# Optimization experiments

Measured on AMD Instinct MI355X. Metric: run time of the kernel, lower is better.

The kernel has to match this reference:

```python
import jax, jax.numpy as jnp
import numpy as np

EPS = 1e-5
N0, K1, K2 = 1000, 500, 100  # node counts fixed by the view() calls in the source


def _conv_bn_relu(x, w, b, g, be):
    # Conv1d(k=1) == per-node linear; BatchNorm1d in training mode over nodes
    h = x @ w.T + b                      # (N, Cout)
    mu = h.mean(0)
    var = h.var(0)                       # biased variance, as torch BN uses
    return jax.nn.relu(g * (h - mu) * jax.lax.rsqrt(var + EPS) + be)


def _linear_relu(x, w, b):
    return jax.nn.relu(x @ w.T + b)


def _sag_pool(x, src, dst, ew, w_rel, w_root, bias, k):
    # SAGPooling with GraphConv scorer (sum aggregation weighted by edge_attr)
    N = x.shape[0]
    agg = jax.ops.segment_sum(ew[:, None] * x[src], dst, num_segments=N)  # (N, C)
    score = agg @ w_rel + x @ w_root + bias                               # (N,)
    top_s, perm = jax.lax.top_k(score, k)
    xk = x[perm] * jnp.tanh(top_s)[:, None]                               # (k, C)
    # re-index edges: keep only edges between surviving nodes (mask, fixed E)
    new_idx = jnp.zeros(N, jnp.int32).at[perm].set(jnp.arange(k, dtype=jnp.int32))
    keep = jnp.zeros(N, bool).at[perm].set(True)
    valid = keep[src] & keep[dst]
    nsrc = jnp.where(valid, new_idx[src], 0)
    ndst = jnp.where(valid, new_idx[dst], 0)
    new_ew = jnp.where(valid, ew, 0.0)  # zero weight == edge removed
    return xk, nsrc, ndst, new_ew


def setup_inputs() -> dict:
    key = jax.random.key(0)
    ks = jax.random.split(key, 32)
    nrm = lambda k, sh, s=0.05: jax.random.normal(k, sh, jnp.float32) * s
    E = 32000
    return {
        "x": jax.random.normal(ks[0], (1, N0, 3), jnp.float32),
        "edge_index": jax.random.randint(ks[1], (2, E), 0, N0, jnp.int32),
        "edge_attr": jax.random.uniform(ks[2], (E,), jnp.float32),
        # input: Conv1d(3,64)+BN
        "w0": nrm(ks[3], (64, 3)), "b0": jnp.zeros(64), "g0": jnp.ones(64), "be0": jnp.zeros(64),
        # mlp_first: Conv1d(64,64)+BN
        "w1": nrm(ks[4], (64, 64)), "b1": jnp.zeros(64), "g1": jnp.ones(64), "be1": jnp.zeros(64),
        # mlp_second: Conv1d(64,128)+BN, Conv1d(128,200)+BN
        "w2a": nrm(ks[5], (128, 64)), "b2a": jnp.zeros(128), "g2a": jnp.ones(128), "be2a": jnp.zeros(128),
        "w2b": nrm(ks[6], (200, 128)), "b2b": jnp.zeros(200), "g2b": jnp.ones(200), "be2b": jnp.zeros(200),
        # mlp_third: Conv1d(200,128), Conv1d(128,2) (no BN)
        "w3a": nrm(ks[7], (128, 200)), "b3a": jnp.zeros(128),
        "w3b": nrm(ks[8], (2, 128)), "b3b": jnp.zeros(2),
        # SAGPooling scorers (GraphConv(in_channels, 1))
        "p1_wrel": nrm(ks[9], (64,)), "p1_wroot": nrm(ks[10], (64,)), "p1_b": jnp.zeros(()),
        "p2_wrel": nrm(ks[11], (200,)), "p2_wroot": nrm(ks[12], (200,)), "p2_b": jnp.zeros(()),
    }


def reference(x, edge_index, edge_attr,
              w0, b0, g0, be0, w1, b1, g1, be1,
              w2a, b2a, g2a, be2a, w2b, b2b, g2b, be2b,
              w3a, b3a, w3b, b3b,
              p1_wrel, p1_wroot, p1_b, p2_wrel, p2_wroot, p2_b):
    h = x.reshape(N0, 3)
    src, dst = edge_index[0], edge_index[1]
    ew = edge_attr.reshape(-1)

    h = _conv_bn_relu(h, w0, b0, g0, be0)      # (1000, 64)
    h = _conv_bn_relu(h, w1, b1, g1, be1)      # (1000, 64)
    h, src, dst, ew = _sag_pool(h, src, dst, ew, p1_wrel, p1_wroot, p1_b, K1)

    h = _conv_bn_relu(h, w2a, b2a, g2a, be2a)  # (500, 128)
    h = _conv_bn_relu(h, w2b, b2b, g2b, be2b)  # (500, 200)
    h, src, dst, ew = _sag_pool(h, src, dst, ew, p2_wrel, p2_wroot, p2_b, K2)

    g = h.max(0)                               # global max pool over 100 nodes -> (200,)
    h3 = _linear_relu(g, w3a, b3a)             # (128,)
    out = _linear_relu(h3, w3b, b3b)           # (2,)
    return jax.nn.log_softmax(out)[None, :]    # (1, 2)
```

## Files before the change

kernel.cpp:

```cpp
#include <hip/hip_runtime.h>
#include <math.h>

#define EPS 1e-5f
#define N0 1000
#define K1 500
#define K2 100
#define NE 32000

__device__ __forceinline__ float bnr(float h, float sc, float sh) {
    float v = fmaf(h, sc, sh);
    return v > 0.f ? v : 0.f;
}

__global__ void k_lin0(const float* __restrict__ x, const float* __restrict__ w0,
                       const float* __restrict__ b0, float* __restrict__ h0,
                       float* __restrict__ psum0) {
    int t = threadIdx.x;
    int c = t & 63, ns = t >> 6;
    int nb = blockIdx.x * 128;
    float wa = w0[c * 3 + 0], wb = w0[c * 3 + 1], wc = w0[c * 3 + 2], bb = b0[c];
    float s = 0.f, q = 0.f;
    for (int j = 0; j < 32; ++j) {
        int n = nb + ns + 4 * j;
        if (n < N0) {
            float h = fmaf(wa, x[n * 3], fmaf(wb, x[n * 3 + 1], fmaf(wc, x[n * 3 + 2], bb)));
            h0[n * 64 + c] = h;
            s += h; q += h * h;
        }
    }
    __shared__ float rs[256], rq[256];
    rs[t] = s; rq[t] = q;
    __syncthreads();
    if (ns == 0) {
        psum0[blockIdx.x * 128 + c]      = rs[c] + rs[c + 64] + rs[c + 128] + rs[c + 192];
        psum0[blockIdx.x * 128 + 64 + c] = rq[c] + rq[c + 64] + rq[c + 128] + rq[c + 192];
    }
}

__global__ void k_lin1(const float* __restrict__ h0, const float* __restrict__ w1,
                       const float* __restrict__ b1v, const float* __restrict__ g0,
                       const float* __restrict__ be0, const float* __restrict__ psum0,
                       float* __restrict__ h1, float* __restrict__ psum1) {
    __shared__ float xs[64][65];
    __shared__ float wsm[64][65];
    __shared__ float sc0[64], sh0[64];
    __shared__ float rs[256], rq[256];
    int t = threadIdx.x;
    int nb = blockIdx.x * 64;
    if (t < 64) {
        float s = 0.f, q = 0.f;
        for (int i = 0; i < 8; ++i) { s += psum0[i * 128 + t]; q += psum0[i * 128 + 64 + t]; }
        float mu = s * (1.f / N0);
        float var = q * (1.f / N0) - mu * mu;
        float sc = g0[t] * rsqrtf(var + EPS);
        sc0[t] = sc; sh0[t] = be0[t] - mu * sc;
    }
    __syncthreads();
    for (int i = 0; i < 16; ++i) {
        int e = t + i * 256;
        int r = e >> 6, cc = e & 63;
        int n = nb + r;
        xs[r][cc] = (n < N0) ? bnr(h0[n * 64 + cc], sc0[cc], sh0[cc]) : 0.f;
        wsm[r][cc] = w1[e];
    }
    __syncthreads();
    int c = t & 63, ns = t >> 6;
    float s = 0.f, q = 0.f;
    for (int j = 0; j < 16; ++j) {
        int ln = ns + 4 * j;
        int n = nb + ln;
        if (n < N0) {
            float acc = b1v[c];
            #pragma unroll
            for (int k = 0; k < 64; ++k) acc = fmaf(xs[ln][k], wsm[c][k], acc);
            h1[n * 64 + c] = acc;
            s += acc; q += acc * acc;
        }
    }
    rs[t] = s; rq[t] = q;
    __syncthreads();
    if (ns == 0) {
        psum1[blockIdx.x * 128 + c]      = rs[c] + rs[c + 64] + rs[c + 128] + rs[c + 192];
        psum1[blockIdx.x * 128 + 64 + c] = rq[c] + rq[c + 64] + rq[c + 128] + rq[c + 192];
    }
}

__global__ void k_score1(const float* __restrict__ h1, const float* __restrict__ psum1,
                         const float* __restrict__ g1, const float* __restrict__ be1,
                         const float* __restrict__ wrel, const float* __restrict__ wroot,
                         const float* __restrict__ pb,
                         float* __restrict__ t1, float* __restrict__ sc1) {
    __shared__ float sc[64], sh[64];
    int t = threadIdx.x;
    if (t < 64) {
        float s = 0.f, q = 0.f;
        for (int i = 0; i < 16; ++i) { s += psum1[i * 128 + t]; q += psum1[i * 128 + 64 + t]; }
        float mu = s * (1.f / N0);
        float var = q * (1.f / N0) - mu * mu;
        float sv = g1[t] * rsqrtf(var + EPS);
        sc[t] = sv; sh[t] = be1[t] - mu * sv;
    }
    __syncthreads();
    int lane = t & 63, w = t >> 6;
    int n = blockIdx.x * 4 + w;
    if (n < N0) {
        float v = bnr(h1[n * 64 + lane], sc[lane], sh[lane]);
        float dr = v * wrel[lane], dt = v * wroot[lane];
        #pragma unroll
        for (int m = 32; m >= 1; m >>= 1) {
            dr += __shfl_xor(dr, m, 64);
            dt += __shfl_xor(dt, m, 64);
        }
        if (lane == 0) { t1[n] = dr; sc1[n] = dt + pb[0]; }
    }
}

__global__ void k_scatter1(const int* __restrict__ ei, const float* __restrict__ ea,
                           const float* __restrict__ t1, float* __restrict__ sc1) {
    __shared__ float acc[N0];
    int t = threadIdx.x;
    for (int i = t; i < N0; i += 256) acc[i] = 0.f;
    __syncthreads();
    for (int e = blockIdx.x * 256 + t; e < NE; e += gridDim.x * 256) {
        float w = ea[e];
        if (w != 0.f) atomicAdd(&acc[ei[NE + e]], w * t1[ei[e]]);
    }
    __syncthreads();
    for (int i = t; i < N0; i += 256) {
        float v = acc[i];
        if (v != 0.f) atomicAdd(&sc1[i], v);
    }
}

__global__ void k_rank1(const float* __restrict__ sc1, const float* __restrict__ h1,
                        const float* __restrict__ psum1, const float* __restrict__ g1,
                        const float* __restrict__ be1,
                        float* __restrict__ xp1, int* __restrict__ keep, int* __restrict__ nidx) {
    __shared__ float ss[N0];
    __shared__ float sc[64], sh[64];
    int t = threadIdx.x;
    if (t < 64) {
        float s = 0.f, q = 0.f;
        for (int i = 0; i < 16; ++i) { s += psum1[i * 128 + t]; q += psum1[i * 128 + 64 + t]; }
        float mu = s * (1.f / N0);
        float var = q * (1.f / N0) - mu * mu;
        float sv = g1[t] * rsqrtf(var + EPS);
        sc[t] = sv; sh[t] = be1[t] - mu * sv;
    }
    for (int i = t; i < N0; i += 256) ss[i] = sc1[i];
    __syncthreads();
    int lane = t & 63, w = t >> 6;
    int n = blockIdx.x * 4 + w;
    if (n < N0) {
        float s = ss[n];
        int r = 0;
        for (int m = lane; m < N0; m += 64) {
            float sm = ss[m];
            r += (sm > s) || (sm == s && m < n);
        }
        #pragma unroll
        for (int msk = 32; msk >= 1; msk >>= 1) r += __shfl_xor(r, msk, 64);
        if (lane == 0) { keep[n] = (r < K1) ? 1 : 0; nidx[n] = (r < K1) ? r : 0; }
        if (r < K1) {
            float tn = tanhf(s);
            xp1[r * 64 + lane] = bnr(h1[n * 64 + lane], sc[lane], sh[lane]) * tn;
        }
    }
}

__global__ void k_lin2a_remap(const float* __restrict__ xp1, const float* __restrict__ w2a,
                              const float* __restrict__ b2a, float* __restrict__ h2a,
                              float* __restrict__ psum2a,
                              const int* __restrict__ ei, const float* __restrict__ ea,
                              const int* __restrict__ keep, const int* __restrict__ nidx,
                              int* __restrict__ nsrc, int* __restrict__ ndst,
                              float* __restrict__ new_ew) {
    __shared__ float xs[64][65];
    __shared__ float wsm[128][65];
    __shared__ float rs[256], rq[256];
    int b = blockIdx.x;
    int t = threadIdx.x;
    if (b < 8) {
        int nb = b * 64;
        for (int i = 0; i < 16; ++i) {
            int e = t + i * 256;
            int r = e >> 6, cc = e & 63;
            int n = nb + r;
            xs[r][cc] = (n < K1) ? xp1[n * 64 + cc] : 0.f;
        }
        for (int i = 0; i < 32; ++i) {
            int e = t + i * 256;
            wsm[e >> 6][e & 63] = w2a[e];
        }
        __syncthreads();
        int c = t & 127, ns = t >> 7;
        float s = 0.f, q = 0.f;
        for (int j = 0; j < 32; ++j) {
            int ln = ns + 2 * j;
            int n = nb + ln;
            if (n < K1) {
                float acc = b2a[c];
                #pragma unroll
                for (int k = 0; k < 64; ++k) acc = fmaf(xs[ln][k], wsm[c][k], acc);
                h2a[n * 128 + c] = acc;
                s += acc; q += acc * acc;
            }
        }
        rs[t] = s; rq[t] = q;
        __syncthreads();
        if (ns == 0) {
            psum2a[b * 256 + c]       = rs[c] + rs[c + 128];
            psum2a[b * 256 + 128 + c] = rq[c] + rq[c + 128];
        }
    } else {
        int e = (b - 8) * 256 + t;
        if (e < NE) {
            int s = ei[e], d = ei[NE + e];
            bool v = keep[s] && keep[d];
            nsrc[e] = v ? nidx[s] : 0;
            ndst[e] = v ? nidx[d] : 0;
            new_ew[e] = v ? ea[e] : 0.f;
        }
    }
}

__global__ void k_lin2b(const float* __restrict__ h2a, const float* __restrict__ psum2a,
                        const float* __restrict__ g2a, const float* __restrict__ be2a,
                        const float* __restrict__ w2b, const float* __restrict__ b2b,
                        float* __restrict__ h2b, float* __restrict__ psum2b) {
    __shared__ float wsm[200][33];
    __shared__ float xs[25][33];
    __shared__ float sc[128], sh[128];
    int t = threadIdx.x;
    if (t < 128) {
        float s = 0.f, q = 0.f;
        for (int i = 0; i < 8; ++i) { s += psum2a[i * 256 + t]; q += psum2a[i * 256 + 128 + t]; }
        float mu = s * (1.f / K1);
        float var = q * (1.f / K1) - mu * mu;
        float sv = g2a[t] * rsqrtf(var + EPS);
        sc[t] = sv; sh[t] = be2a[t] - mu * sv;
    }
    __syncthreads();
    int nb = blockIdx.x * 25;
    float acc[25];
    if (t < 200) {
        float bb = b2b[t];
        #pragma unroll
        for (int r = 0; r < 25; ++r) acc[r] = bb;
    }
    for (int kt = 0; kt < 4; ++kt) {
        int k0 = kt * 32;
        __syncthreads();
        for (int e = t; e < 200 * 32; e += 256) {
            int r = e >> 5, k = e & 31;
            wsm[r][k] = w2b[r * 128 + k0 + k];
        }
        for (int e = t; e < 25 * 32; e += 256) {
            int r = e >> 5, k = e & 31;
            int n = nb + r;
            xs[r][k] = bnr(h2a[n * 128 + k0 + k], sc[k0 + k], sh[k0 + k]);
        }
        __syncthreads();
        if (t < 200) {
            for (int k = 0; k < 32; ++k) {
                float wv = wsm[t][k];
                #pragma unroll
                for (int r = 0; r < 25; ++r) acc[r] = fmaf(xs[r][k], wv, acc[r]);
            }
        }
    }
    if (t < 200) {
        float s = 0.f, q = 0.f;
        #pragma unroll
        for (int r = 0; r < 25; ++r) {
            int n = nb + r;
            h2b[n * 200 + t] = acc[r];
            s += acc[r]; q += acc[r] * acc[r];
        }
        psum2b[blockIdx.x * 400 + t]       = s;
        psum2b[blockIdx.x * 400 + 200 + t] = q;
    }
}

__global__ void k_score2(const float* __restrict__ h2b, const float* __restrict__ psum2b,
                         const float* __restrict__ g2b, const float* __restrict__ be2b,
                         const float* __restrict__ wrel, const float* __restrict__ wroot,
                         const float* __restrict__ pb,
                         float* __restrict__ t2, float* __restrict__ sc2) {
    __shared__ float sc[200], sh[200];
    int t = threadIdx.x;
    if (t < 200) {
        float s = 0.f, q = 0.f;
        for (int i = 0; i < 20; ++i) { s += psum2b[i * 400 + t]; q += psum2b[i * 400 + 200 + t]; }
        float mu = s * (1.f / K1);
        float var = q * (1.f / K1) - mu * mu;
        float sv = g2b[t] * rsqrtf(var + EPS);
        sc[t] = sv; sh[t] = be2b[t] - mu * sv;
    }
    __syncthreads();
    int lane = t & 63, w = t >> 6;
    int n = blockIdx.x * 4 + w;
    if (n < K1) {
        float dr = 0.f, dt = 0.f;
        #pragma unroll
        for (int j = 0; j < 4; ++j) {
            int ch = lane + 64 * j;
            if (ch < 200) {
                float v = bnr(h2b[n * 200 + ch], sc[ch], sh[ch]);
                dr = fmaf(v, wrel[ch], dr);
                dt = fmaf(v, wroot[ch], dt);
            }
        }
        #pragma unroll
        for (int m = 32; m >= 1; m >>= 1) {
            dr += __shfl_xor(dr, m, 64);
            dt += __shfl_xor(dt, m, 64);
        }
        if (lane == 0) { t2[n] = dr; sc2[n] = dt + pb[0]; }
    }
}

__global__ void k_scatter2(const int* __restrict__ nsrc, const int* __restrict__ ndst,
                           const float* __restrict__ new_ew, const float* __restrict__ t2,
                           float* __restrict__ sc2) {
    __shared__ float acc[K1];
    int t = threadIdx.x;
    for (int i = t; i < K1; i += 256) acc[i] = 0.f;
    __syncthreads();
    for (int e = blockIdx.x * 256 + t; e < NE; e += gridDim.x * 256) {
        float w = new_ew[e];
        if (w != 0.f) atomicAdd(&acc[ndst[e]], w * t2[nsrc[e]]);
    }
    __syncthreads();
    for (int i = t; i < K1; i += 256) {
        float v = acc[i];
        if (v != 0.f) atomicAdd(&sc2[i], v);
    }
}

__global__ void k_rank2(const float* __restrict__ sc2v, const float* __restrict__ h2b,
                        const float* __restrict__ psum2b, const float* __restrict__ g2b,
                        const float* __restrict__ be2b, float* __restrict__ xp2) {
    __shared__ float ss[K1];
    __shared__ float sc[200], sh[200];
    int t = threadIdx.x;
    if (t < 200) {
        float s = 0.f, q = 0.f;
        for (int i = 0; i < 20; ++i) { s += psum2b[i * 400 + t]; q += psum2b[i * 400 + 200 + t]; }
        float mu = s * (1.f / K1);
        float var = q * (1.f / K1) - mu * mu;
        float sv = g2b[t] * rsqrtf(var + EPS);
        sc[t] = sv; sh[t] = be2b[t] - mu * sv;
    }
    for (int i = t; i < K1; i += 256) ss[i] = sc2v[i];
    __syncthreads();
    int lane = t & 63, w = t >> 6;
    int n = blockIdx.x * 4 + w;
    if (n < K1) {
        float s = ss[n];
        int r = 0;
        for (int m = lane; m < K1; m += 64) {
            float sm = ss[m];
            r += (sm > s) || (sm == s && m < n);
        }
        #pragma unroll
        for (int msk = 32; msk >= 1; msk >>= 1) r += __shfl_xor(r, msk, 64);
        if (r < K2) {
            float tn = tanhf(s);
            #pragma unroll
            for (int j = 0; j < 4; ++j) {
                int ch = lane + 64 * j;
                if (ch < 200)
                    xp2[r * 200 + ch] = bnr(h2b[n * 200 + ch], sc[ch], sh[ch]) * tn;
            }
        }
    }
}

__global__ void k_final(const float* __restrict__ xp2, const float* __restrict__ w3a,
                        const float* __restrict__ b3a, const float* __restrict__ w3b,
                        const float* __restrict__ b3b, float* __restrict__ out) {
    __shared__ float g[200];
    __shared__ float buf[64][201];
    __shared__ float part[256];
    __shared__ float h3[128];
    __shared__ float o[2];
    int t = threadIdx.x;
    if (t < 200) {
        float m = -1e30f;
        for (int n = 0; n < K2; ++n) m = fmaxf(m, xp2[n * 200 + t]);
        g[t] = m;
    }
    __syncthreads();
    int lane = t & 63, q = t >> 6;
    for (int chunk = 0; chunk < 2; ++chunk) {
        int r0 = chunk * 64;
        __syncthreads();
        for (int e = t; e < 64 * 200; e += 256) {
            int r = e / 200, j = e - r * 200;
            buf[r][j] = w3a[r0 * 200 + e];
        }
        __syncthreads();
        float p = 0.f;
        for (int j = q * 50; j < q * 50 + 50; ++j) p = fmaf(buf[lane][j], g[j], p);
        part[t] = p;
        __syncthreads();
        if (t < 64) {
            float a = part[t] + part[t + 64] + part[t + 128] + part[t + 192] + b3a[r0 + t];
            h3[r0 + t] = fmaxf(a, 0.f);
        }
    }
    __syncthreads();
    if (t < 128) {
        int ow = t >> 6;
        float p = w3b[ow * 128 + lane] * h3[lane] + w3b[ow * 128 + 64 + lane] * h3[64 + lane];
        #pragma unroll
        for (int m = 32; m >= 1; m >>= 1) p += __shfl_xor(p, m, 64);
        if (lane == 0) o[ow] = fmaxf(p + b3b[ow], 0.f);
    }
    __syncthreads();
    if (t == 0) {
        float m = fmaxf(o[0], o[1]);
        float l = m + logf(expf(o[0] - m) + expf(o[1] - m));
        out[0] = o[0] - l;
        out[1] = o[1] - l;
    }
}

extern "C" void kernel_launch(void* const* d_in, const int* in_sizes, int n_in,
                              void* d_out, int out_size, void* d_ws, size_t ws_size,
                              hipStream_t stream) {
    const float* x    = (const float*)d_in[0];
    const int*   ei   = (const int*)d_in[1];
    const float* ea   = (const float*)d_in[2];
    const float* w0   = (const float*)d_in[3];
    const float* b0   = (const float*)d_in[4];
    const float* g0   = (const float*)d_in[5];
    const float* be0  = (const float*)d_in[6];
    const float* w1   = (const float*)d_in[7];
    const float* b1   = (const float*)d_in[8];
    const float* g1   = (const float*)d_in[9];
    const float* be1  = (const float*)d_in[10];
    const float* w2a  = (const float*)d_in[11];
    const float* b2a  = (const float*)d_in[12];
    const float* g2a  = (const float*)d_in[13];
    const float* be2a = (const float*)d_in[14];
    const float* w2b  = (const float*)d_in[15];
    const float* b2b  = (const float*)d_in[16];
    const float* g2b  = (const float*)d_in[17];
    const float* be2b = (const float*)d_in[18];
    const float* w3a  = (const float*)d_in[19];
    const float* b3a  = (const float*)d_in[20];
    const float* w3b  = (const float*)d_in[21];
    const float* b3b  = (const float*)d_in[22];
    const float* p1_wrel  = (const float*)d_in[23];
    const float* p1_wroot = (const float*)d_in[24];
    const float* p1_b     = (const float*)d_in[25];
    const float* p2_wrel  = (const float*)d_in[26];
    const float* p2_wroot = (const float*)d_in[27];
    const float* p2_b     = (const float*)d_in[28];

    float* ws = (float*)d_ws;
    float* h0     = ws;
    float* h1     = ws + 64000;
    float* psum0  = ws + 128000;
    float* psum1  = ws + 129024;
    float* psum2a = ws + 131072;
    float* psum2b = ws + 133120;
    float* t1     = ws + 141120;
    float* sc1    = ws + 142120;
    float* xp1    = ws + 143120;
    float* h2a    = ws + 175120;
    float* h2b    = ws + 239120;
    float* t2     = ws + 339120;
    float* sc2    = ws + 339620;
    float* xp2    = ws + 340120;
    int*   keep   = (int*)(ws + 360120);
    int*   nidx   = (int*)(ws + 361120);
    int*   nsrc   = (int*)(ws + 362120);
    int*   ndst   = (int*)(ws + 394120);
    float* new_ew = ws + 426120;

    float* out = (float*)d_out;

    k_lin0<<<8, 256, 0, stream>>>(x, w0, b0, h0, psum0);
    k_lin1<<<16, 256, 0, stream>>>(h0, w1, b1, g0, be0, psum0, h1, psum1);
    k_score1<<<250, 256, 0, stream>>>(h1, psum1, g1, be1, p1_wrel, p1_wroot, p1_b, t1, sc1);
    k_scatter1<<<16, 256, 0, stream>>>(ei, ea, t1, sc1);
    k_rank1<<<250, 256, 0, stream>>>(sc1, h1, psum1, g1, be1, xp1, keep, nidx);
    k_lin2a_remap<<<133, 256, 0, stream>>>(xp1, w2a, b2a, h2a, psum2a,
                                           ei, ea, keep, nidx, nsrc, ndst, new_ew);
    k_lin2b<<<20, 256, 0, stream>>>(h2a, psum2a, g2a, be2a, w2b, b2b, h2b, psum2b);
    k_score2<<<125, 256, 0, stream>>>(h2b, psum2b, g2b, be2b, p2_wrel, p2_wroot, p2_b, t2, sc2);
    k_scatter2<<<16, 256, 0, stream>>>(nsrc, ndst, new_ew, t2, sc2);
    k_rank2<<<125, 256, 0, stream>>>(sc2, h2b, psum2b, g2b, be2b, xp2);
    k_final<<<1, 256, 0, stream>>>(xp2, w3a, b3a, w3b, b3b, out);
}
```

Baseline: 130.3 us.

## Fuse graph pipeline into four kernels with redundant per-block pooling

Collapses eleven kernel launches into four. Each block of the first kernel recomputes the layer-0 batch-norm statistics itself. Each of the eight blocks in the pool1+lin2a kernel redundantly computes scores, edge scatter and ranking for all nodes in shared memory, then does its slice of the edge remap and the lin2a GEMM. The second pooling, ranking, global max and MLP head all run in one 1024-thread block. This removes launch overhead and global round-trips, but adds duplicated work across blocks and a serial O(N²) per-thread rank loop.

```diff
diff --git a/kernel.cpp b/kernel.cpp
--- a/kernel.cpp
+++ b/kernel.cpp
@@ -3,8 +3,8 @@
 
 #define EPS 1e-5f
 #define N0 1000
-#define K1 500
-#define K2 100
+#define NK1 500
+#define NK2 100
 #define NE 32000
 
 __device__ __forceinline__ float bnr(float h, float sc, float sh) {
@@ -12,65 +12,61 @@
     return v > 0.f ? v : 0.f;
 }
 
-__global__ void k_lin0(const float* __restrict__ x, const float* __restrict__ w0,
-                       const float* __restrict__ b0, float* __restrict__ h0,
-                       float* __restrict__ psum0) {
-    int t = threadIdx.x;
-    int c = t & 63, ns = t >> 6;
-    int nb = blockIdx.x * 128;
-    float wa = w0[c * 3 + 0], wb = w0[c * 3 + 1], wc = w0[c * 3 + 2], bb = b0[c];
-    float s = 0.f, q = 0.f;
-    for (int j = 0; j < 32; ++j) {
-        int n = nb + ns + 4 * j;
-        if (n < N0) {
-            float h = fmaf(wa, x[n * 3], fmaf(wb, x[n * 3 + 1], fmaf(wc, x[n * 3 + 2], bb)));
-            h0[n * 64 + c] = h;
-            s += h; q += h * h;
-        }
-    }
-    __shared__ float rs[256], rq[256];
-    rs[t] = s; rq[t] = q;
-    __syncthreads();
-    if (ns == 0) {
-        psum0[blockIdx.x * 128 + c]      = rs[c] + rs[c + 64] + rs[c + 128] + rs[c + 192];
-        psum0[blockIdx.x * 128 + 64 + c] = rq[c] + rq[c + 64] + rq[c + 128] + rq[c + 192];
-    }
-}
-
-__global__ void k_lin1(const float* __restrict__ h0, const float* __restrict__ w1,
-                       const float* __restrict__ b1v, const float* __restrict__ g0,
-                       const float* __restrict__ be0, const float* __restrict__ psum0,
-                       float* __restrict__ h1, float* __restrict__ psum1) {
-    __shared__ float xs[64][65];
-    __shared__ float wsm[64][65];
+__global__ __launch_bounds__(256) void k_lin01(
+        const float* __restrict__ x, const float* __restrict__ w0,
+        const float* __restrict__ b0, const float* __restrict__ g0,
+        const float* __restrict__ be0, const float* __restrict__ w1,
+        const float* __restrict__ b1, float* __restrict__ h1,
+        float* __restrict__ psum1) {
+    __shared__ float xs[64][65], wsm[64][65];
     __shared__ float sc0[64], sh0[64];
     __shared__ float rs[256], rq[256];
-    int t = threadIdx.x;
-    int nb = blockIdx.x * 64;
-    if (t < 64) {
+    const int t = threadIdx.x, b = blockIdx.x;
+    const int c = t & 63, ns = t >> 6;
+    const int nb = b * 64;
+
+    {
+        float wa = w0[c * 3], wb = w0[c * 3 + 1], wc = w0[c * 3 + 2], bb = b0[c];
         float s = 0.f, q = 0.f;
-        for (int i = 0; i < 8; ++i) { s += psum0[i * 128 + t]; q += psum0[i * 128 + 64 + t]; }
-        float mu = s * (1.f / N0);
-        float var = q * (1.f / N0) - mu * mu;
-        float sc = g0[t] * rsqrtf(var + EPS);
-        sc0[t] = sc; sh0[t] = be0[t] - mu * sc;
-    }
-    __syncthreads();
+        for (int n = ns; n < N0; n += 4) {
+            float h = fmaf(wa, x[n * 3], fmaf(wb, x[n * 3 + 1], fmaf(wc, x[n * 3 + 2], bb)));
+            s += h; q += h * h;
+        }
+        rs[t] = s; rq[t] = q;
+        __syncthreads();
+        if (ns == 0) {
+            float S = rs[c] + rs[c + 64] + rs[c + 128] + rs[c + 192];
+            float Q = rq[c] + rq[c + 64] + rq[c + 128] + rq[c + 192];
+            float mu = S * (1.f / N0);
+            float var = Q * (1.f / N0) - mu * mu;
+            float sv = g0[c] * rsqrtf(var + EPS);
+            sc0[c] = sv; sh0[c] = be0[c] - mu * sv;
+        }
+        __syncthreads();
+    }
+
     for (int i = 0; i < 16; ++i) {
         int e = t + i * 256;
         int r = e >> 6, cc = e & 63;
         int n = nb + r;
-        xs[r][cc] = (n < N0) ? bnr(h0[n * 64 + cc], sc0[cc], sh0[cc]) : 0.f;
+        float v = 0.f;
+        if (n < N0) {
+            float h = fmaf(w0[cc * 3], x[n * 3],
+                      fmaf(w0[cc * 3 + 1], x[n * 3 + 1],
+                      fmaf(w0[cc * 3 + 2], x[n * 3 + 2], b0[cc])));
+            v = bnr(h, sc0[cc], sh0[cc]);
+        }
+        xs[r][cc] = v;
         wsm[r][cc] = w1[e];
     }
     __syncthreads();
-    int c = t & 63, ns = t >> 6;
+
     float s = 0.f, q = 0.f;
     for (int j = 0; j < 16; ++j) {
         int ln = ns + 4 * j;
         int n = nb + ln;
         if (n < N0) {
-            float acc = b1v[c];
+            float acc = b1[c];
             #pragma unroll
             for (int k = 0; k < 64; ++k) acc = fmaf(xs[ln][k], wsm[c][k], acc);
             h1[n * 64 + c] = acc;
@@ -80,154 +76,131 @@
     rs[t] = s; rq[t] = q;
     __syncthreads();
     if (ns == 0) {
-        psum1[blockIdx.x * 128 + c]      = rs[c] + rs[c + 64] + rs[c + 128] + rs[c + 192];
-        psum1[blockIdx.x * 128 + 64 + c] = rq[c] + rq[c + 64] + rq[c + 128] + rq[c + 192];
-    }
-}
-
-__global__ void k_score1(const float* __restrict__ h1, const float* __restrict__ psum1,
-                         const float* __restrict__ g1, const float* __restrict__ be1,
-                         const float* __restrict__ wrel, const float* __restrict__ wroot,
-                         const float* __restrict__ pb,
-                         float* __restrict__ t1, float* __restrict__ sc1) {
-    __shared__ float sc[64], sh[64];
-    int t = threadIdx.x;
+        psum1[b * 128 + c]      = rs[c] + rs[c + 64] + rs[c + 128] + rs[c + 192];
+        psum1[b * 128 + 64 + c] = rq[c] + rq[c + 64] + rq[c + 128] + rq[c + 192];
+    }
+}
+
+__global__ __launch_bounds__(1024) void k_pool1_lin2a(
+        const float* __restrict__ h1, const float* __restrict__ psum1,
+        const float* __restrict__ g1, const float* __restrict__ be1,
+        const float* __restrict__ wrel, const float* __restrict__ wroot,
+        const float* __restrict__ pb,
+        const int* __restrict__ ei, const float* __restrict__ ea,
+        const float* __restrict__ w2a, const float* __restrict__ b2a,
+        float* __restrict__ h2a, float* __restrict__ psum2a,
+        int* __restrict__ nsrc, int* __restrict__ ndst,
+        float* __restrict__ new_ew) {
+    union U {
+        struct { float ss[N0], tt[N0], acc[N0]; int rk[N0]; } A;
+        struct { float xs[64][65], wsm[128][65], rs[1024], rq[1024]; } C;
+    };
+    __shared__ U u;
+    __shared__ float bsc[64], bsh[64];
+    __shared__ int pn[NK1];
+    __shared__ float th[NK1];
+    const int t = threadIdx.x, b = blockIdx.x;
+    const int lane = t & 63, w = t >> 6;
+
     if (t < 64) {
         float s = 0.f, q = 0.f;
         for (int i = 0; i < 16; ++i) { s += psum1[i * 128 + t]; q += psum1[i * 128 + 64 + t]; }
         float mu = s * (1.f / N0);
         float var = q * (1.f / N0) - mu * mu;
         float sv = g1[t] * rsqrtf(var + EPS);
-        sc[t] = sv; sh[t] = be1[t] - mu * sv;
-    }
-    __syncthreads();
-    int lane = t & 63, w = t >> 6;
-    int n = blockIdx.x * 4 + w;
-    if (n < N0) {
-        float v = bnr(h1[n * 64 + lane], sc[lane], sh[lane]);
+        bsc[t] = sv; bsh[t] = be1[t] - mu * sv;
+    }
+    for (int i = t; i < N0; i += 1024) u.A.acc[i] = 0.f;
+    __syncthreads();
+
+    for (int n = w; n < N0; n += 16) {
+        float v = bnr(h1[n * 64 + lane], bsc[lane], bsh[lane]);
         float dr = v * wrel[lane], dt = v * wroot[lane];
         #pragma unroll
         for (int m = 32; m >= 1; m >>= 1) {
             dr += __shfl_xor(dr, m, 64);
             dt += __shfl_xor(dt, m, 64);
         }
-        if (lane == 0) { t1[n] = dr; sc1[n] = dt + pb[0]; }
-    }
-}
-
-__global__ void k_scatter1(const int* __restrict__ ei, const float* __restrict__ ea,
-                           const float* __restrict__ t1, float* __restrict__ sc1) {
-    __shared__ float acc[N0];
-    int t = threadIdx.x;
-    for (int i = t; i < N0; i += 256) acc[i] = 0.f;
-    __syncthreads();
-    for (int e = blockIdx.x * 256 + t; e < NE; e += gridDim.x * 256) {
-        float w = ea[e];
-        if (w != 0.f) atomicAdd(&acc[ei[NE + e]], w * t1[ei[e]]);
-    }
-    __syncthreads();
-    for (int i = t; i < N0; i += 256) {
-        float v = acc[i];
-        if (v != 0.f) atomicAdd(&sc1[i], v);
-    }
-}
-
-__global__ void k_rank1(const float* __restrict__ sc1, const float* __restrict__ h1,
-                        const float* __restrict__ psum1, const float* __restrict__ g1,
-                        const float* __restrict__ be1,
-                        float* __restrict__ xp1, int* __restrict__ keep, int* __restrict__ nidx) {
-    __shared__ float ss[N0];
-    __shared__ float sc[64], sh[64];
-    int t = threadIdx.x;
-    if (t < 64) {
-        float s = 0.f, q = 0.f;
-        for (int i = 0; i < 16; ++i) { s += psum1[i * 128 + t]; q += psum1[i * 128 + 64 + t]; }
-        float mu = s * (1.f / N0);
-        float var = q * (1.f / N0) - mu * mu;
-        float sv = g1[t] * rsqrtf(var + EPS);
-        sc[t] = sv; sh[t] = be1[t] - mu * sv;
-    }
-    for (int i = t; i < N0; i += 256) ss[i] = sc1[i];
-    __syncthreads();
-    int lane = t & 63, w = t >> 6;
-    int n = blockIdx.x * 4 + w;
-    if (n < N0) {
-        float s = ss[n];
+        if (lane == 0) { u.A.tt[n] = dr; u.A.ss[n] = dt + pb[0]; }
+    }
+    __syncthreads();
+
+    for (int e = t; e < NE; e += 1024) {
+        float ew = ea[e];
+        if (ew != 0.f) atomicAdd(&u.A.acc[ei[NE + e]], ew * u.A.tt[ei[e]]);
+    }
+    __syncthreads();
+    for (int i = t; i < N0; i += 1024) u.A.ss[i] += u.A.acc[i];
+    __syncthreads();
+
+    if (t < N0) {
+        float s = u.A.ss[t];
         int r = 0;
-        for (int m = lane; m < N0; m += 64) {
-            float sm = ss[m];
-            r += (sm > s) || (sm == s && m < n);
-        }
-        #pragma unroll
-        for (int msk = 32; msk >= 1; msk >>= 1) r += __shfl_xor(r, msk, 64);
-        if (lane == 0) { keep[n] = (r < K1) ? 1 : 0; nidx[n] = (r < K1) ? r : 0; }
-        if (r < K1) {
-            float tn = tanhf(s);
-            xp1[r * 64 + lane] = bnr(h1[n * 64 + lane], sc[lane], sh[lane]) * tn;
-        }
-    }
-}
-
-__global__ void k_lin2a_remap(const float* __restrict__ xp1, const float* __restrict__ w2a,
-                              const float* __restrict__ b2a, float* __restrict__ h2a,
-                              float* __restrict__ psum2a,
-                              const int* __restrict__ ei, const float* __restrict__ ea,
-                              const int* __restrict__ keep, const int* __restrict__ nidx,
-                              int* __restrict__ nsrc, int* __restrict__ ndst,
-                              float* __restrict__ new_ew) {
-    __shared__ float xs[64][65];
-    __shared__ float wsm[128][65];
-    __shared__ float rs[256], rq[256];
-    int b = blockIdx.x;
-    int t = threadIdx.x;
-    if (b < 8) {
-        int nb = b * 64;
-        for (int i = 0; i < 16; ++i) {
-            int e = t + i * 256;
-            int r = e >> 6, cc = e & 63;
-            int n = nb + r;
-            xs[r][cc] = (n < K1) ? xp1[n * 64 + cc] : 0.f;
-        }
-        for (int i = 0; i < 32; ++i) {
-            int e = t + i * 256;
-            wsm[e >> 6][e & 63] = w2a[e];
-        }
-        __syncthreads();
-        int c = t & 127, ns = t >> 7;
-        float s = 0.f, q = 0.f;
-        for (int j = 0; j < 32; ++j) {
-            int ln = ns + 2 * j;
-            int n = nb + ln;
-            if (n < K1) {
-                float acc = b2a[c];
-                #pragma unroll
-                for (int k = 0; k < 64; ++k) acc = fmaf(xs[ln][k], wsm[c][k], acc);
-                h2a[n * 128 + c] = acc;
-                s += acc; q += acc * acc;
-            }
-        }
-        rs[t] = s; rq[t] = q;
-        __syncthreads();
-        if (ns == 0) {
-            psum2a[b * 256 + c]       = rs[c] + rs[c + 128];
-            psum2a[b * 256 + 128 + c] = rq[c] + rq[c + 128];
-        }
-    } else {
-        int e = (b - 8) * 256 + t;
-        if (e < NE) {
-            int s = ei[e], d = ei[NE + e];
-            bool v = keep[s] && keep[d];
-            nsrc[e] = v ? nidx[s] : 0;
-            ndst[e] = v ? nidx[d] : 0;
-            new_ew[e] = v ? ea[e] : 0.f;
-        }
-    }
-}
-
-__global__ void k_lin2b(const float* __restrict__ h2a, const float* __restrict__ psum2a,
-                        const float* __restrict__ g2a, const float* __restrict__ be2a,
-                        const float* __restrict__ w2b, const float* __restrict__ b2b,
-                        float* __restrict__ h2b, float* __restrict__ psum2b) {
+        for (int m = 0; m < N0; ++m) {
+            float smv = u.A.ss[m];
+            r += (smv > s) || (smv == s && m < t);
+        }
+        u.A.rk[t] = r;
+        if (r < NK1) { pn[r] = t; th[r] = tanhf(s); }
+    }
+    __syncthreads();
+
+    for (int e = b * 4000 + t; e < (b + 1) * 4000; e += 1024) {
+        int s_ = ei[e], d_ = ei[NE + e];
+        int rs_ = u.A.rk[s_], rd_ = u.A.rk[d_];
+        bool v = (rs_ < NK1) && (rd_ < NK1);
+        nsrc[e] = v ? rs_ : 0;
+        ndst[e] = v ? rd_ : 0;
+        new_ew[e] = v ? ea[e] : 0.f;
+    }
+    __syncthreads();
+
+    const int nb = b * 63;
+    const int nrows = (NK1 - nb) < 63 ? (NK1 - nb) : 63;
+    for (int idx = t; idx < 64 * 64; idx += 1024) {
+        int r = idx >> 6, c = idx & 63;
+        float v = 0.f;
+        if (r < nrows) {
+            int n = pn[nb + r];
+            v = bnr(h1[n * 64 + c], bsc[c], bsh[c]) * th[nb + r];
+        }
+        u.C.xs[r][c] = v;
+    }
+    for (int idx = t; idx < 128 * 64; idx += 1024) {
+        int c = idx >> 6, k = idx & 63;
+        u.C.wsm[c][k] = w2a[idx];
+    }
+    __syncthreads();
+
+    const int c = t & 127, slot = t >> 7;
+    float s = 0.f, q = 0.f;
+    #pragma unroll
+    for (int j = 0; j < 8; ++j) {
+        int r = slot + 8 * j;
+        if (r < nrows) {
+            float acc = b2a[c];
+            #pragma unroll
+            for (int k = 0; k < 64; ++k) acc = fmaf(u.C.xs[r][k], u.C.wsm[c][k], acc);
+            h2a[(nb + r) * 128 + c] = acc;
+            s += acc; q += acc * acc;
+        }
+    }
+    u.C.rs[t] = s; u.C.rq[t] = q;
+    __syncthreads();
+    if (slot == 0) {
+        float S = 0.f, Q = 0.f;
+        #pragma unroll
+        for (int j = 0; j < 8; ++j) { S += u.C.rs[c + 128 * j]; Q += u.C.rq[c + 128 * j]; }
+        psum2a[b * 256 + c]       = S;
+        psum2a[b * 256 + 128 + c] = Q;
+    }
+}
+
+__global__ __launch_bounds__(256) void k_lin2b(
+        const float* __restrict__ h2a, const float* __restrict__ psum2a,
+        const float* __restrict__ g2a, const float* __restrict__ be2a,
+        const float* __restrict__ w2b, const float* __restrict__ b2b,
+        float* __restrict__ h2b, float* __restrict__ psum2b) {
     __shared__ float wsm[200][33];
     __shared__ float xs[25][33];
     __shared__ float sc[128], sh[128];
@@ -235,19 +208,17 @@
     if (t < 128) {
         float s = 0.f, q = 0.f;
         for (int i = 0; i < 8; ++i) { s += psum2a[i * 256 + t]; q += psum2a[i * 256 + 128 + t]; }
-        float mu = s * (1.f / K1);
-        float var = q * (1.f / K1) - mu * mu;
+        float mu = s * (1.f / NK1);
+        float var = q * (1.f / NK1) - mu * mu;
         float sv = g2a[t] * rsqrtf(var + EPS);
         sc[t] = sv; sh[t] = be2a[t] - mu * sv;
     }
     __syncthreads();
     int nb = blockIdx.x * 25;
     float acc[25];
-    if (t < 200) {
-        float bb = b2b[t];
-        #pragma unroll
-        for (int r = 0; r < 25; ++r) acc[r] = bb;
-    }
+    float bb = (t < 200) ? b2b[t] : 0.f;
+    #pragma unroll
+    for (int r = 0; r < 25; ++r) acc[r] = bb;
     for (int kt = 0; kt < 4; ++kt) {
         int k0 = kt * 32;
         __syncthreads();
@@ -257,8 +228,7 @@
         }
         for (int e = t; e < 25 * 32; e += 256) {
             int r = e >> 5, k = e & 31;
-            int n = nb + r;
-            xs[r][k] = bnr(h2a[n * 128 + k0 + k], sc[k0 + k], sh[k0 + k]);
+            xs[r][k] = bnr(h2a[(nb + r) * 128 + k0 + k], sc[k0 + k], sh[k0 + k]);
         }
         __syncthreads();
         if (t < 200) {
@@ -273,8 +243,7 @@
         float s = 0.f, q = 0.f;
         #pragma unroll
         for (int r = 0; r < 25; ++r) {
-            int n = nb + r;
-            h2b[n * 200 + t] = acc[r];
+            h2b[(nb + r) * 200 + t] = acc[r];
             s += acc[r]; q += acc[r] * acc[r];
         }
         psum2b[blockIdx.x * 400 + t]       = s;
@@ -282,31 +251,44 @@
     }
 }
 
-__global__ void k_score2(const float* __restrict__ h2b, const float* __restrict__ psum2b,
-                         const float* __restrict__ g2b, const float* __restrict__ be2b,
-                         const float* __restrict__ wrel, const float* __restrict__ wroot,
-                         const float* __restrict__ pb,
-                         float* __restrict__ t2, float* __restrict__ sc2) {
-    __shared__ float sc[200], sh[200];
-    int t = threadIdx.x;
+__global__ __launch_bounds__(1024) void k_pool2_final(
+        const float* __restrict__ h2b, const float* __restrict__ psum2b,
+        const float* __restrict__ g2b, const float* __restrict__ be2b,
+        const float* __restrict__ wrel, const float* __restrict__ wroot,
+        const float* __restrict__ pb,
+        const int* __restrict__ nsrc, const int* __restrict__ ndst,
+        const float* __restrict__ new_ew,
+        const float* __restrict__ w3a, const float* __restrict__ b3a,
+        const float* __restrict__ w3b, const float* __restrict__ b3b,
+        float* __restrict__ out) {
+    __shared__ float bsc[200], bsh[200];
+    __shared__ float ss[NK1], tt[NK1], acc[NK1];
+    __shared__ int pn[NK2];
+    __shared__ float th[NK2];
+    __shared__ float gp[16 * 200];
+    __shared__ float g[200], h3[128], o[2];
+    const int t = threadIdx.x;
+    const int lane = t & 63, w = t >> 6;
+
     if (t < 200) {
         float s = 0.f, q = 0.f;
         for (int i = 0; i < 20; ++i) { s += psum2b[i * 400 + t]; q += psum2b[i * 400 + 200 + t]; }
-        float mu = s * (1.f / K1);
-        float var = q * (1.f / K1) - mu * mu;
+        float mu = s * (1.f / NK1);
+        float var = q * (1.f / NK1) - mu * mu;
         float sv = g2b[t] * rsqrtf(var + EPS);
-        sc[t] = sv; sh[t] = be2b[t] - mu * sv;
-    }
-    __syncthreads();
-    int lane = t & 63, w = t >> 6;
-    int n = blockIdx.x * 4 + w;
-    if (n < K1) {
+        bsc[t] = sv; bsh[t] = be2b[t] - mu * sv;
+    }
+    for (int i = t; i < NK1; i += 1024) acc[i] = 0.f;
+    for (int i = t; i < 16 * 200; i += 1024) gp[i] = -1e30f;
+    __syncthreads();
+
+    for (int n = w; n < NK1; n += 16) {
         float dr = 0.f, dt = 0.f;
         #pragma unroll
         for (int j = 0; j < 4; ++j) {
             int ch = lane + 64 * j;
             if (ch < 200) {
-                float v = bnr(h2b[n * 200 + ch], sc[ch], sh[ch]);
+                float v = bnr(h2b[n * 200 + ch], bsc[ch], bsh[ch]);
                 dr = fmaf(v, wrel[ch], dr);
                 dt = fmaf(v, wroot[ch], dt);
             }
@@ -316,104 +298,67 @@
             dr += __shfl_xor(dr, m, 64);
             dt += __shfl_xor(dt, m, 64);
         }
-        if (lane == 0) { t2[n] = dr; sc2[n] = dt + pb[0]; }
-    }
-}
-
-__global__ void k_scatter2(const int* __restrict__ nsrc, const int* __restrict__ ndst,
-                           const float* __restrict__ new_ew, const float* __restrict__ t2,
-                           float* __restrict__ sc2) {
-    __shared__ float acc[K1];
-    int t = threadIdx.x;
-    for (int i = t; i < K1; i += 256) acc[i] = 0.f;
-    __syncthreads();
-    for (int e = blockIdx.x * 256 + t; e < NE; e += gridDim.x * 256) {
-        float w = new_ew[e];
-        if (w != 0.f) atomicAdd(&acc[ndst[e]], w * t2[nsrc[e]]);
-    }
-    __syncthreads();
-    for (int i = t; i < K1; i += 256) {
-        float v = acc[i];
-        if (v != 0.f) atomicAdd(&sc2[i], v);
-    }
-}
-
-__global__ void k_rank2(const float* __restrict__ sc2v, const float* __restrict__ h2b,
-                        const float* __restrict__ psum2b, const float* __restrict__ g2b,
-                        const float* __restrict__ be2b, float* __restrict__ xp2) {
-    __shared__ float ss[K1];
-    __shared__ float sc[200], sh[200];
-    int t = threadIdx.x;
+        if (lane == 0) { tt[n] = dr; ss[n] = dt + pb[0]; }
+    }
+    __syncthreads();
+
+    for (int e = t; e < NE; e += 1024) {
+        float ew = new_ew[e];
+        if (ew != 0.f) atomicAdd(&acc[ndst[e]], ew * tt[nsrc[e]]);
+    }
+    __syncthreads();
+    for (int i = t; i < NK1; i += 1024) ss[i] += acc[i];
+    __syncthreads();
+
+    if (t < NK1) {
+        float s = ss[t];
+        int r = 0;
+        for (int m = 0; m < NK1; ++m) {
+            float smv = ss[m];
+            r += (smv > s) || (smv == s && m < t);
+        }
+        if (r < NK2) { pn[r] = t; th[r] = tanhf(s); }
+    }
+    __syncthreads();
+
+    for (int j = w; j < NK2; j += 16) {
+        int n = pn[j];
+        float tn = th[j];
+        #pragma unroll
+        for (int jj = 0; jj < 4; ++jj) {
+            int ch = lane + 64 * jj;
+            if (ch < 200) {
+                float v = bnr(h2b[n * 200 + ch], bsc[ch], bsh[ch]) * tn;
+                gp[w * 200 + ch] = fmaxf(gp[w * 200 + ch], v);
+            }
+        }
+    }
+    __syncthreads();
     if (t < 200) {
-        float s = 0.f, q = 0.f;
-        for (int i = 0; i < 20; ++i) { s += psum2b[i * 400 + t]; q += psum2b[i * 400 + 200 + t]; }
-        float mu = s * (1.f / K1);
-        float var = q * (1.f / K1) - mu * mu;
-        float sv = g2b[t] * rsqrtf(var + EPS);
-        sc[t] = sv; sh[t] = be2b[t] - mu * sv;
-    }
-    for (int i = t; i < K1; i += 256) ss[i] = sc2v[i];
-    __syncthreads();
-    int lane = t & 63, w = t >> 6;
-    int n = blockIdx.x * 4 + w;
-    if (n < K1) {
-        float s = ss[n];
-        int r = 0;
-        for (int m = lane; m < K1; m += 64) {
-            float sm = ss[m];
-            r += (sm > s) || (sm == s && m < n);
-        }
-        #pragma unroll
-        for (int msk = 32; msk >= 1; msk >>= 1) r += __shfl_xor(r, msk, 64);
-        if (r < K2) {
-            float tn = tanhf(s);
-            #pragma unroll
-            for (int j = 0; j < 4; ++j) {
-                int ch = lane + 64 * j;
-                if (ch < 200)
-                    xp2[r * 200 + ch] = bnr(h2b[n * 200 + ch], sc[ch], sh[ch]) * tn;
-            }
-        }
-    }
-}
-
-__global__ void k_final(const float* __restrict__ xp2, const float* __restrict__ w3a,
-                        const float* __restrict__ b3a, const float* __restrict__ w3b,
-                        const float* __restrict__ b3b, float* __restrict__ out) {
-    __shared__ float g[200];
-    __shared__ float buf[64][201];
-    __shared__ float part[256];
-    __shared__ float h3[128];
-    __shared__ float o[2];
-    int t = threadIdx.x;
-    if (t < 200) {
-        float m = -1e30f;
-        for (int n = 0; n < K2; ++n) m = fmaxf(m, xp2[n * 200 + t]);
+        float m = gp[t];
+        #pragma unroll
+        for (int i = 1; i < 16; ++i) m = fmaxf(m, gp[i * 200 + t]);
         g[t] = m;
     }
     __syncthreads();
-    int lane = t & 63, q = t >> 6;
-    for (int chunk = 0; chunk < 2; ++chunk) {
-        int r0 = chunk * 64;
-        __syncthreads();
-        for (int e = t; e < 64 * 200; e += 256) {
-            int r = e / 200, j = e - r * 200;
-            buf[r][j] = w3a[r0 * 200 + e];
-        }
-        __syncthreads();
+
+    for (int r = w; r < 128; r += 16) {
         float p = 0.f;
-        for (int j = q * 50; j < q * 50 + 50; ++j) p = fmaf(buf[lane][j], g[j], p);
-        part[t] = p;
-        __syncthreads();
-        if (t < 64) {
-            float a = part[t] + part[t + 64] + part[t + 128] + part[t + 192] + b3a[r0 + t];
-            h3[r0 + t] = fmaxf(a, 0.f);
-        }
-    }
-    __syncthreads();
+        #pragma unroll
+        for (int jj = 0; jj < 4; ++jj) {
+            int ch = lane + 64 * jj;
+            if (ch < 200) p = fmaf(w3a[r * 200 + ch], g[ch], p);
+        }
+        #pragma unroll
+        for (int m = 32; m >= 1; m >>= 1) p += __shfl_xor(p, m, 64);
+        if (lane == 0) h3[r] = fmaxf(p + b3a[r], 0.f);
+    }
+    __syncthreads();
+
     if (t < 128) {
         int ow = t >> 6;
-        float p = w3b[ow * 128 + lane] * h3[lane] + w3b[ow * 128 + 64 + lane] * h3[64 + lane];
+        float p = w3b[ow * 128 + lane] * h3[lane]
+                + w3b[ow * 128 + 64 + lane] * h3[64 + lane];
         #pragma unroll
         for (int m = 32; m >= 1; m >>= 1) p += __shfl_xor(p, m, 64);
         if (lane == 0) o[ow] = fmaxf(p + b3b[ow], 0.f);
@@ -461,38 +406,26 @@
     const float* p2_b     = (const float*)d_in[28];
 
     float* ws = (float*)d_ws;
-    float* h0     = ws;
-    float* h1     = ws + 64000;
-    float* psum0  = ws + 128000;
-    float* psum1  = ws + 129024;
-    float* psum2a = ws + 131072;
-    float* psum2b = ws + 133120;
-    float* t1     = ws + 141120;
-    float* sc1    = ws + 142120;
-    float* xp1    = ws + 143120;
-    float* h2a    = ws + 175120;
-    float* h2b    = ws + 239120;
-    float* t2     = ws + 339120;
-    float* sc2    = ws + 339620;
-    float* xp2    = ws + 340120;
-    int*   keep   = (int*)(ws + 360120);
-    int*   nidx   = (int*)(ws + 361120);
-    int*   nsrc   = (int*)(ws + 362120);
-    int*   ndst   = (int*)(ws + 394120);
-    float* new_ew = ws + 426120;
+    float* h1     = ws;
+    float* psum1  = ws + 64000;
+    float* h2a    = ws + 66048;
+    float* psum2a = ws + 130048;
+    float* h2b    = ws + 132096;
+    float* psum2b = ws + 232096;
+    int*   nsrc   = (int*)(ws + 240096);
+    int*   ndst   = (int*)(ws + 272096);
+    float* new_ew = ws + 304096;
 
     float* out = (float*)d_out;
 
-    k_lin0<<<8, 256, 0, stream>>>(x, w0, b0, h0, psum0);
-    k_lin1<<<16, 256, 0, stream>>>(h0, w1, b1, g0, be0, psum0, h1, psum1);
-    k_score1<<<250, 256, 0, stream>>>(h1, psum1, g1, be1, p1_wrel, p1_wroot, p1_b, t1, sc1);
-    k_scatter1<<<16, 256, 0, stream>>>(ei, ea, t1, sc1);
-    k_rank1<<<250, 256, 0, stream>>>(sc1, h1, psum1, g1, be1, xp1, keep, nidx);
-    k_lin2a_remap<<<133, 256, 0, stream>>>(xp1, w2a, b2a, h2a, psum2a,
-                                           ei, ea, keep, nidx, nsrc, ndst, new_ew);
+    k_lin01<<<16, 256, 0, stream>>>(x, w0, b0, g0, be0, w1, b1, h1, psum1);
+    k_pool1_lin2a<<<8, 1024, 0, stream>>>(h1, psum1, g1, be1,
+                                          p1_wrel, p1_wroot, p1_b,
+                                          ei, ea, w2a, b2a,
+                                          h2a, psum2a, nsrc, ndst, new_ew);
     k_lin2b<<<20, 256, 0, stream>>>(h2a, psum2a, g2a, be2a, w2b, b2b, h2b, psum2b);
-    k_score2<<<125, 256, 0, stream>>>(h2b, psum2b, g2b, be2b, p2_wrel, p2_wroot, p2_b, t2, sc2);
-    k_scatter2<<<16, 256, 0, stream>>>(nsrc, ndst, new_ew, t2, sc2);
-    k_rank2<<<125, 256, 0, stream>>>(sc2, h2b, psum2b, g2b, be2b, xp2);
-    k_final<<<1, 256, 0, stream>>>(xp2, w3a, b3a, w3b, b3b, out);
-}
+    k_pool2_final<<<1, 1024, 0, stream>>>(h2b, psum2b, g2b, be2b,
+                                          p2_wrel, p2_wroot, p2_b,
+                                          nsrc, ndst, new_ew,
+                                          w3a, b3a, w3b, b3b, out);
+}
```

Result: slower. 279.9 us (+114.8%).
